# Optimization experiments

Hardware: AMD Instinct MI355X
Metric: run time of the kernel (lower is better)

Reference implementation:

```python
import jax, jax.numpy as jnp
import numpy as np

B, C, H, W = 4, 64, 224, 224
MAX_SEG = 256       # max superpixel label -> segment buffer size 257
MAX_SEG_REF = 256


def _superfeatures(feat, labels, num_seg):
    """scatter_max segment pooling over interior pixels.
    feat [B,C,H,W], labels [B,1,H,W] int -> [B,C,num_seg]."""
    b, c = feat.shape[:2]
    src = feat[:, :, 1:-1, 1:-1].reshape(b, c, -1)   # [B,C,P]
    idx = labels[:, 0, 1:-1, 1:-1].reshape(b, -1)    # [B,P]

    def one(s, i):
        m = jax.ops.segment_max(s.T, i, num_segments=num_seg)  # [S,C]
        return jnp.where(jnp.isneginf(m), 0.0, m).T            # empty segments -> 0

    return jax.vmap(one)(src, idx)                   # [B,C,S]


def _chan_norm(x, eps=1e-5):
    # per-superpixel: subtract channel mean, divide by channel L2 norm (torch dim=1)
    xm = x - jnp.mean(x, axis=1, keepdims=True)
    return xm / (jnp.linalg.norm(xm, axis=1, keepdims=True) + eps)


def setup_inputs():
    key = jax.random.key(0)
    ks = jax.random.split(key, 11)
    rn = lambda k, sh: jax.random.normal(k, sh, dtype=jnp.float32)
    return {
        "feat_target": rn(ks[0], (B, C, H, W)),
        "feat_ref": rn(ks[1], (B, C, H, W)),
        "feat_rgb_ref": rn(ks[2], (B, C, H, W)),
        "Wq": rn(ks[3], (C, C)) * 0.1, "bq": rn(ks[4], (C,)) * 0.1,
        "Wk": rn(ks[5], (C, C)) * 0.1, "bk": rn(ks[6], (C,)) * 0.1,
        "Wv": rn(ks[7], (C, C)) * 0.1, "bv": rn(ks[8], (C,)) * 0.1,
        "label_mask_target": jax.random.randint(ks[9], (B, 1, H, W), 0, MAX_SEG + 1, dtype=jnp.int32),
        "label_mask_ref": jax.random.randint(ks[10], (B, 1, H, W), 0, MAX_SEG_REF + 1, dtype=jnp.int32),
        "max_segments": MAX_SEG,
        "max_segments_ref": MAX_SEG_REF,
    }


def reference(feat_target, feat_ref, feat_rgb_ref, Wq, bq, Wk, bk, Wv, bv,
              label_mask_target, label_mask_ref, max_segments, max_segments_ref):
    S_t = max_segments + 1
    S_r = max_segments_ref + 1
    b, c, h, w = feat_target.shape

    # Superfeatures: segment pooling (scatter_max)
    enc_t = _superfeatures(feat_target, label_mask_target, S_t)   # [B,C,S_t]
    enc_r = _superfeatures(feat_ref, label_mask_ref, S_r)         # [B,C,S_r]
    enc_v = _superfeatures(feat_rgb_ref, label_mask_ref, S_r)     # [B,C,S_r]

    # per-sample variable lengths (label_target / label_ref in the torch loop)
    n_t = jnp.max(label_mask_target.reshape(b, -1), axis=1) + 1
    n_r = jnp.max(label_mask_ref.reshape(b, -1), axis=1) + 1
    tmask = jnp.arange(S_t)[None, :] < n_t[:, None]               # [B,S_t]
    rmask = jnp.arange(S_r)[None, :] < n_r[:, None]               # [B,S_r]

    # Superattention_conv (batched over the original per-sample loop)
    q = jnp.einsum('oc,bcn->bon', Wq, _chan_norm(enc_t)) + bq[None, :, None]
    k = jnp.einsum('oc,bcm->bom', Wk, _chan_norm(enc_r)) + bk[None, :, None]
    v = jnp.einsum('oc,bcm->bom', Wv, enc_v) + bv[None, :, None]  # value conv on raw rgb feats

    sim = jnp.einsum('bcn,bcm->bnm', q, k) / 0.01                 # temperature 0.01
    sim = jnp.where(rmask[:, None, :], sim, -jnp.inf)             # mask invalid ref cols
    attn = jax.nn.softmax(sim, axis=2) * tmask[:, :, None]        # softmax dim=2, zero pad rows

    wg = jnp.einsum('bnm,bcm->bcn', attn, v)                      # [B,C,S_t] (transposed wg_ref)

    # Unpool_features: gather back to pixel grid
    idx = jnp.broadcast_to(label_mask_target.reshape(b, 1, -1), (b, c, h * w))
    unpool = jnp.take_along_axis(wg, idx, axis=2).reshape(b, c, h, w)
    return unpool
```

## Files before the change

### kernel.cpp

```cpp
#include <hip/hip_runtime.h>
#include <math.h>

#define BB 4
#define CC 64
#define HH 224
#define WW 224
#define HWW (HH*WW)
#define SS 257
#define CPB 8
#define NRC 16
#define RPC 14
#define ENCW (3*BB*CC*SS)

__device__ __forceinline__ unsigned fkey(float f) {
    unsigned u = __float_as_uint(f);
    return (u & 0x80000000u) ? ~u : (u | 0x80000000u);
}
__device__ __forceinline__ float funkey(unsigned k) {
    return (k & 0x80000000u) ? __uint_as_float(k & 0x7FFFFFFFu) : __uint_as_float(~k);
}
#define SENT 0x007FFFFFu

__global__ __launch_bounds__(256) void init_kernel(unsigned* __restrict__ enc,
                                                   int* __restrict__ nmax) {
    int i = blockIdx.x * 256 + threadIdx.x;
    if (i < ENCW / 4) ((uint4*)enc)[i] = make_uint4(SENT, SENT, SENT, SENT);
    if (i < 2 * BB) nmax[i] = 0;
}

__global__ __launch_bounds__(256) void pool_kernel(
    const float* __restrict__ fT, const float* __restrict__ fR,
    const float* __restrict__ fV,
    const int* __restrict__ labT, const int* __restrict__ labR,
    unsigned* __restrict__ enc, int* __restrict__ nmax)
{
    __shared__ unsigned seg[CPB * SS];
    __shared__ int wmax[4];
    const int cg = blockIdx.x, rc = blockIdx.y;
    const int z = blockIdx.z >> 2, b = blockIdx.z & 3;
    const float* src = (z == 0) ? fT : (z == 1) ? fR : fV;
    const int*   lab = (z == 0) ? labT : labR;

    for (int i = threadIdx.x; i < CPB * SS; i += 256) seg[i] = SENT;
    __syncthreads();

    const int h0 = rc * RPC;
    const int h1 = min(222, h0 + RPC);
    const int ngroups = (h1 - h0) * 56;

    const int*    lp  = lab + (size_t)b * HWW;
    const int4*   lp4 = (const int4*)lp;
    const float4* fp4 = (const float4*)(src + (size_t)(b * CC + cg * CPB) * HWW);
    const int PS4 = HWW / 4;

    const bool do_nmax = (cg == 0) && (z < 2);
    int lmax = -1;

    for (int gi = threadIdx.x; gi < ngroups; gi += 256) {
        int h = gi / 56;
        int g = gi - h * 56;
        int idx4 = (h0 + h + 1) * 56 + g;
        int4   l  = lp4[idx4];
        float4 f0 = fp4[idx4          ];
        float4 f1 = fp4[idx4 + 1 * PS4];
        float4 f2 = fp4[idx4 + 2 * PS4];
        float4 f3 = fp4[idx4 + 3 * PS4];
        float4 f4 = fp4[idx4 + 4 * PS4];
        float4 f5 = fp4[idx4 + 5 * PS4];
        float4 f6 = fp4[idx4 + 6 * PS4];
        float4 f7 = fp4[idx4 + 7 * PS4];
        if (do_nmax)
            lmax = max(lmax, max(max(l.x, l.y), max(l.z, l.w)));
        const bool mx = (g != 0), mw = (g != 55);
#define PROC(F, CCN) do { \
        unsigned kx = fkey(F.x), ky = fkey(F.y), kz = fkey(F.z), kw = fkey(F.w); \
        unsigned* sg = seg + (CCN) * SS; \
        if (mx && kx > sg[l.x]) atomicMax(&sg[l.x], kx); \
        if (ky > sg[l.y]) atomicMax(&sg[l.y], ky); \
        if (kz > sg[l.z]) atomicMax(&sg[l.z], kz); \
        if (mw && kw > sg[l.w]) atomicMax(&sg[l.w], kw); } while (0)
        PROC(f0, 0); PROC(f1, 1); PROC(f2, 2); PROC(f3, 3);
        PROC(f4, 4); PROC(f5, 5); PROC(f6, 6); PROC(f7, 7);
#undef PROC
    }

    if (do_nmax && threadIdx.x < 56) {
        if (rc == 0) {
            int4 l = lp4[threadIdx.x];
            lmax = max(lmax, max(max(l.x, l.y), max(l.z, l.w)));
        }
        if (rc == NRC - 1) {
            int4 l = lp4[223 * 56 + threadIdx.x];
            lmax = max(lmax, max(max(l.x, l.y), max(l.z, l.w)));
        }
    }
    #pragma unroll
    for (int o = 32; o; o >>= 1) lmax = max(lmax, __shfl_xor(lmax, o, 64));
    if ((threadIdx.x & 63) == 0) wmax[threadIdx.x >> 6] = lmax;
    __syncthreads();
    if (do_nmax && threadIdx.x == 0) {
        int m = max(max(wmax[0], wmax[1]), max(wmax[2], wmax[3]));
        atomicMax(&nmax[z * BB + b], m + 1);
    }

    unsigned* gp = enc + (size_t)((z * BB + b) * CC + cg * CPB) * SS;
    for (int i = threadIdx.x; i < CPB * SS; i += 256) {
        unsigned k = seg[i];
        if (k != SENT) atomicMax(&gp[i], k);
    }
}

__global__ __launch_bounds__(512) void qkv_kernel(
    const unsigned* __restrict__ enc,
    const float* __restrict__ Wq, const float* __restrict__ bq,
    const float* __restrict__ Wk, const float* __restrict__ bk,
    const float* __restrict__ Wv, const float* __restrict__ bv,
    float* __restrict__ qkv)
{
    const int z = blockIdx.z, b = blockIdx.y;
    const int wid = threadIdx.x >> 6, lane = threadIdx.x & 63;
    const int n = blockIdx.x * 8 + wid;
    if (n >= SS) return;

    const float* Wm = (z == 0) ? Wq : (z == 1) ? Wk : Wv;
    const float* bm = (z == 0) ? bq : (z == 1) ? bk : bv;
    const unsigned* ep = enc + (size_t)((z * BB + b) * CC) * SS + n;

    unsigned kraw = ep[(size_t)lane * SS];
    float x = (kraw == SENT) ? 0.0f : funkey(kraw);
    if (z != 2) {
        float s = x;
        for (int o = 32; o; o >>= 1) s += __shfl_xor(s, o, 64);
        float xm = x - s * (1.0f / 64.0f);
        float s2 = xm * xm;
        for (int o = 32; o; o >>= 1) s2 += __shfl_xor(s2, o, 64);
        x = xm / (sqrtf(s2) + 1e-5f);
    }
    float acc = bm[lane];
    #pragma unroll
    for (int cI = 0; cI < 64; ++cI) {
        float xc = __shfl(x, cI, 64);
        acc = fmaf(Wm[lane * 64 + cI], xc, acc);
    }
    qkv[(size_t)((z * BB + b) * SS + n) * CC + lane] = acc;
}

__global__ __launch_bounds__(256) void attn_kernel(
    const float* __restrict__ qkv, const int* __restrict__ nmax,
    float* __restrict__ wg)
{
    const int n = blockIdx.x, b = blockIdx.y, t = threadIdx.x;
    __shared__ float qs[CC];
    __shared__ float sim[512];
    __shared__ float red[256];
    __shared__ float pv[4][64];

    const int nT = nmax[b], nR = nmax[BB + b];
    float* wp = wg + (size_t)(b * SS + n) * CC;
    if (n >= nT) {
        if (t < CC) wp[t] = 0.0f;
        return;
    }
    const float* q = qkv + (size_t)(0 * BB + b) * SS * CC;
    const float* k = qkv + (size_t)(1 * BB + b) * SS * CC;
    const float* v = qkv + (size_t)(2 * BB + b) * SS * CC;

    if (t < CC) qs[t] = q[(size_t)n * CC + t];
    sim[t] = -INFINITY;
    sim[t + 256] = -INFINITY;
    __syncthreads();

    for (int m = t; m < SS; m += 256) {
        float s = -INFINITY;
        if (m < nR) {
            const float4* kr = (const float4*)(k + (size_t)m * CC);
            float acc = 0.0f;
            #pragma unroll
            for (int i = 0; i < 16; ++i) {
                float4 kv = kr[i];
                acc += qs[4*i+0]*kv.x + qs[4*i+1]*kv.y + qs[4*i+2]*kv.z + qs[4*i+3]*kv.w;
            }
            s = acc * 100.0f;
        }
        sim[m] = s;
    }
    __syncthreads();

    red[t] = fmaxf(sim[t], sim[t + 256]);
    __syncthreads();
    for (int s = 128; s > 0; s >>= 1) {
        if (t < s) red[t] = fmaxf(red[t], red[t + s]);
        __syncthreads();
    }
    const float mx = red[0];
    __syncthreads();

    float psum = 0.0f;
    for (int m = t; m < SS; m += 256) {
        float e = expf(sim[m] - mx);
        sim[m] = e;
        psum += e;
    }
    red[t] = psum;
    __syncthreads();
    for (int s = 128; s > 0; s >>= 1) {
        if (t < s) red[t] += red[t + s];
        __syncthreads();
    }
    const float rdenom = 1.0f / red[0];

    const int g = t >> 6, c = t & 63;
    float acc = 0.0f;
    for (int m = g; m < SS; m += 4)
        acc = fmaf(sim[m], v[(size_t)m * CC + c], acc);
    pv[g][c] = acc;
    __syncthreads();
    if (t < CC)
        wp[t] = (pv[0][t] + pv[1][t] + pv[2][t] + pv[3][t]) * rdenom;
}

__global__ __launch_bounds__(256) void unpool_kernel(
    const float* __restrict__ wg, const int* __restrict__ labT,
    float* __restrict__ out)
{
    const int idx = blockIdx.x * 256 + threadIdx.x;
    if (idx >= BB * HWW) return;
    const int b = idx / HWW, hw = idx - b * HWW;
    const int l = labT[idx];
    const float4* row = (const float4*)(wg + (size_t)(b * SS + l) * CC);
    float* op = out + (size_t)b * CC * HWW + hw;
    #pragma unroll
    for (int i = 0; i < 16; ++i) {
        float4 r = row[i];
        op[(size_t)(4*i+0) * HWW] = r.x;
        op[(size_t)(4*i+1) * HWW] = r.y;
        op[(size_t)(4*i+2) * HWW] = r.z;
        op[(size_t)(4*i+3) * HWW] = r.w;
    }
}

extern "C" void kernel_launch(void* const* d_in, const int* in_sizes, int n_in,
                              void* d_out, int out_size, void* d_ws, size_t ws_size,
                              hipStream_t stream) {
    (void)in_sizes; (void)n_in; (void)out_size; (void)ws_size;
    const float* fT  = (const float*)d_in[0];
    const float* fR  = (const float*)d_in[1];
    const float* fV  = (const float*)d_in[2];
    const float* Wq  = (const float*)d_in[3];
    const float* bq  = (const float*)d_in[4];
    const float* Wk  = (const float*)d_in[5];
    const float* bk  = (const float*)d_in[6];
    const float* Wv  = (const float*)d_in[7];
    const float* bv  = (const float*)d_in[8];
    const int* labT  = (const int*)d_in[9];
    const int* labR  = (const int*)d_in[10];
    float* out = (float*)d_out;

    unsigned* enc = (unsigned*)d_ws;
    float* qkv  = (float*)d_ws + ENCW;
    float* wg   = qkv + 3 * BB * CC * SS;
    int*   nmax = (int*)(wg + BB * CC * SS);

    init_kernel<<<(ENCW / 4 + 255) / 256, 256, 0, stream>>>(enc, nmax);
    pool_kernel<<<dim3(CPB, NRC, 12), 256, 0, stream>>>(fT, fR, fV, labT, labR, enc, nmax);
    qkv_kernel<<<dim3((SS + 7) / 8, BB, 3), 512, 0, stream>>>(enc, Wq, bq, Wk, bk, Wv, bv, qkv);
    attn_kernel<<<dim3(SS, BB), 256, 0, stream>>>(qkv, nmax, wg);
    unpool_kernel<<<(BB * HWW + 255) / 256, 256, 0, stream>>>(wg, labT, out);
}
```

Measured before the change: 94.35 us.

## Double-buffer pool loads with inline asm global loads and vmcnt waits

Rewrites the pooling loop as a fixed four-iteration, double-buffered pipeline. Two register sets are filled by inline-asm global_load_dwordx4 using scalar base pointers, and partial s_waitcnt vmcnt lets the next batch of loads stay in flight while the current one runs the shared-memory atomic max. Out-of-range groups are clamped to the last valid group, and the border label reads for nmax are issued before the barrier so they overlap the shared-memory init. This costs more VGPRs, which may lower occupancy, and the inline asm adds fragility.

```diff
diff --git a/kernel.cpp b/kernel.cpp
--- a/kernel.cpp
+++ b/kernel.cpp
@@ -12,6 +12,9 @@
 #define RPC 14
 #define ENCW (3*BB*CC*SS)
 
+typedef float f32x4 __attribute__((ext_vector_type(4)));
+typedef int   i32x4 __attribute__((ext_vector_type(4)));
+
 __device__ __forceinline__ unsigned fkey(float f) {
     unsigned u = __float_as_uint(f);
     return (u & 0x80000000u) ? ~u : (u | 0x80000000u);
@@ -27,6 +30,58 @@
     if (i < ENCW / 4) ((uint4*)enc)[i] = make_uint4(SENT, SENT, SENT, SENT);
     if (i < 2 * BB) nmax[i] = 0;
 }
+
+#define SETA aF0,aF1,aF2,aF3,aF4,aF5,aF6,aF7,aL
+#define SETB bF0,bF1,bF2,bF3,bF4,bF5,bF6,bF7,bL
+
+#define ISSUE_(OFF, F0,F1,F2,F3,F4,F5,F6,F7,LL) \
+    asm volatile( \
+        "global_load_dwordx4 %0, %9, %10\n\t" \
+        "global_load_dwordx4 %1, %9, %11\n\t" \
+        "global_load_dwordx4 %2, %9, %12\n\t" \
+        "global_load_dwordx4 %3, %9, %13\n\t" \
+        "global_load_dwordx4 %4, %9, %14\n\t" \
+        "global_load_dwordx4 %5, %9, %15\n\t" \
+        "global_load_dwordx4 %6, %9, %16\n\t" \
+        "global_load_dwordx4 %7, %9, %17\n\t" \
+        "global_load_dwordx4 %8, %9, %18\n\t" \
+        : "=&v"(F0), "=&v"(F1), "=&v"(F2), "=&v"(F3), \
+          "=&v"(F4), "=&v"(F5), "=&v"(F6), "=&v"(F7), "=&v"(LL) \
+        : "v"(OFF), "s"(q0), "s"(q1), "s"(q2), "s"(q3), \
+          "s"(q4), "s"(q5), "s"(q6), "s"(q7), "s"(ql))
+#define ISSUE(OFF, SET) ISSUE_(OFF, SET)
+
+#define WAITB_(NSTR, F0,F1,F2,F3,F4,F5,F6,F7,LL) \
+    asm volatile("s_waitcnt vmcnt(" NSTR ")" \
+        : "+v"(F0), "+v"(F1), "+v"(F2), "+v"(F3), \
+          "+v"(F4), "+v"(F5), "+v"(F6), "+v"(F7), "+v"(LL))
+#define WAITB(NSTR, SET) WAITB_(NSTR, SET)
+
+#define PR1(F, J, LX, LY, LZ, LW, MX, MW) do { \
+    unsigned kx = fkey(F[0]), ky = fkey(F[1]), kz = fkey(F[2]), kw = fkey(F[3]); \
+    unsigned* sg = seg + (J) * SS; \
+    if ((MX) && kx > sg[LX]) atomicMax(&sg[LX], kx); \
+    if (ky > sg[LY]) atomicMax(&sg[LY], ky); \
+    if (kz > sg[LZ]) atomicMax(&sg[LZ], kz); \
+    if ((MW) && kw > sg[LW]) atomicMax(&sg[LW], kw); \
+} while (0)
+
+#define PROCB_(IT, F0,F1,F2,F3,F4,F5,F6,F7,LL) do { \
+    int gi = min((IT) * 256 + t, NGR - 1); \
+    int g  = gi % 56; \
+    bool mx = (g != 0), mw = (g != 55); \
+    if (do_nmax) lmax = max(lmax, max(max(LL[0], LL[1]), max(LL[2], LL[3]))); \
+    int lx = LL[0], ly = LL[1], lz = LL[2], lw = LL[3]; \
+    PR1(F0, 0, lx, ly, lz, lw, mx, mw); \
+    PR1(F1, 1, lx, ly, lz, lw, mx, mw); \
+    PR1(F2, 2, lx, ly, lz, lw, mx, mw); \
+    PR1(F3, 3, lx, ly, lz, lw, mx, mw); \
+    PR1(F4, 4, lx, ly, lz, lw, mx, mw); \
+    PR1(F5, 5, lx, ly, lz, lw, mx, mw); \
+    PR1(F6, 6, lx, ly, lz, lw, mx, mw); \
+    PR1(F7, 7, lx, ly, lz, lw, mx, mw); \
+} while (0)
+#define PROCB(IT, SET) PROCB_(IT, SET)
 
 __global__ __launch_bounds__(256) void pool_kernel(
     const float* __restrict__ fT, const float* __restrict__ fR,
@@ -38,73 +93,66 @@
     __shared__ int wmax[4];
     const int cg = blockIdx.x, rc = blockIdx.y;
     const int z = blockIdx.z >> 2, b = blockIdx.z & 3;
+    const int t = threadIdx.x;
     const float* src = (z == 0) ? fT : (z == 1) ? fR : fV;
     const int*   lab = (z == 0) ? labT : labR;
 
-    for (int i = threadIdx.x; i < CPB * SS; i += 256) seg[i] = SENT;
-    __syncthreads();
-
-    const int h0 = rc * RPC;
-    const int h1 = min(222, h0 + RPC);
-    const int ngroups = (h1 - h0) * 56;
-
-    const int*    lp  = lab + (size_t)b * HWW;
-    const int4*   lp4 = (const int4*)lp;
-    const float4* fp4 = (const float4*)(src + (size_t)(b * CC + cg * CPB) * HWW);
-    const int PS4 = HWW / 4;
+    const float* pf = src + (size_t)(b * CC + cg * CPB) * HWW;
+    const int*   lp = lab + (size_t)b * HWW;
+    unsigned long long q0 = (unsigned long long)(uintptr_t)(pf + 0 * HWW);
+    unsigned long long q1 = (unsigned long long)(uintptr_t)(pf + 1 * HWW);
+    unsigned long long q2 = (unsigned long long)(uintptr_t)(pf + 2 * HWW);
+    unsigned long long q3 = (unsigned long long)(uintptr_t)(pf + 3 * HWW);
+    unsigned long long q4 = (unsigned long long)(uintptr_t)(pf + 4 * HWW);
+    unsigned long long q5 = (unsigned long long)(uintptr_t)(pf + 5 * HWW);
+    unsigned long long q6 = (unsigned long long)(uintptr_t)(pf + 6 * HWW);
+    unsigned long long q7 = (unsigned long long)(uintptr_t)(pf + 7 * HWW);
+    unsigned long long ql = (unsigned long long)(uintptr_t)lp;
+
+    for (int i = t; i < CPB * SS; i += 256) seg[i] = SENT;
 
     const bool do_nmax = (cg == 0) && (z < 2);
     int lmax = -1;
-
-    for (int gi = threadIdx.x; gi < ngroups; gi += 256) {
-        int h = gi / 56;
-        int g = gi - h * 56;
-        int idx4 = (h0 + h + 1) * 56 + g;
-        int4   l  = lp4[idx4];
-        float4 f0 = fp4[idx4          ];
-        float4 f1 = fp4[idx4 + 1 * PS4];
-        float4 f2 = fp4[idx4 + 2 * PS4];
-        float4 f3 = fp4[idx4 + 3 * PS4];
-        float4 f4 = fp4[idx4 + 4 * PS4];
-        float4 f5 = fp4[idx4 + 5 * PS4];
-        float4 f6 = fp4[idx4 + 6 * PS4];
-        float4 f7 = fp4[idx4 + 7 * PS4];
-        if (do_nmax)
-            lmax = max(lmax, max(max(l.x, l.y), max(l.z, l.w)));
-        const bool mx = (g != 0), mw = (g != 55);
-#define PROC(F, CCN) do { \
-        unsigned kx = fkey(F.x), ky = fkey(F.y), kz = fkey(F.z), kw = fkey(F.w); \
-        unsigned* sg = seg + (CCN) * SS; \
-        if (mx && kx > sg[l.x]) atomicMax(&sg[l.x], kx); \
-        if (ky > sg[l.y]) atomicMax(&sg[l.y], ky); \
-        if (kz > sg[l.z]) atomicMax(&sg[l.z], kz); \
-        if (mw && kw > sg[l.w]) atomicMax(&sg[l.w], kw); } while (0)
-        PROC(f0, 0); PROC(f1, 1); PROC(f2, 2); PROC(f3, 3);
-        PROC(f4, 4); PROC(f5, 5); PROC(f6, 6); PROC(f7, 7);
-#undef PROC
-    }
-
-    if (do_nmax && threadIdx.x < 56) {
-        if (rc == 0) {
-            int4 l = lp4[threadIdx.x];
-            lmax = max(lmax, max(max(l.x, l.y), max(l.z, l.w)));
-        }
-        if (rc == NRC - 1) {
-            int4 l = lp4[223 * 56 + threadIdx.x];
-            lmax = max(lmax, max(max(l.x, l.y), max(l.z, l.w)));
-        }
-    }
+    if (do_nmax && t < 112) {
+        const i32x4* l4 = (const i32x4*)lp;
+        i32x4 v = (t < 56) ? l4[t] : l4[223 * 56 + (t - 56)];
+        lmax = max(lmax, max(max(v[0], v[1]), max(v[2], v[3])));
+    }
+    __syncthreads();
+
+    const int h0i = rc * RPC;
+    const int NGR = (min(222, h0i + RPC) - h0i) * 56;
+    const unsigned base4 = (unsigned)((h0i + 1) * 56);
+
+    f32x4 aF0, aF1, aF2, aF3, aF4, aF5, aF6, aF7; i32x4 aL;
+    f32x4 bF0, bF1, bF2, bF3, bF4, bF5, bF6, bF7; i32x4 bL;
+
+    unsigned vo0 = (base4 + (unsigned)min(0 * 256 + t, NGR - 1)) * 16u;
+    unsigned vo1 = (base4 + (unsigned)min(1 * 256 + t, NGR - 1)) * 16u;
+    unsigned vo2 = (base4 + (unsigned)min(2 * 256 + t, NGR - 1)) * 16u;
+    unsigned vo3 = (base4 + (unsigned)min(3 * 256 + t, NGR - 1)) * 16u;
+
+    ISSUE(vo0, SETA);
+    ISSUE(vo1, SETB);  WAITB("9", SETA);
+    PROCB(0, SETA);
+    ISSUE(vo2, SETA);  WAITB("9", SETB);
+    PROCB(1, SETB);
+    ISSUE(vo3, SETB);  WAITB("9", SETA);
+    PROCB(2, SETA);
+    WAITB("0", SETB);
+    PROCB(3, SETB);
+
     #pragma unroll
     for (int o = 32; o; o >>= 1) lmax = max(lmax, __shfl_xor(lmax, o, 64));
-    if ((threadIdx.x & 63) == 0) wmax[threadIdx.x >> 6] = lmax;
-    __syncthreads();
-    if (do_nmax && threadIdx.x == 0) {
+    if ((t & 63) == 0) wmax[t >> 6] = lmax;
+    __syncthreads();
+    if (do_nmax && t == 0) {
         int m = max(max(wmax[0], wmax[1]), max(wmax[2], wmax[3]));
         atomicMax(&nmax[z * BB + b], m + 1);
     }
 
     unsigned* gp = enc + (size_t)((z * BB + b) * CC + cg * CPB) * SS;
-    for (int i = threadIdx.x; i < CPB * SS; i += 256) {
+    for (int i = t; i < CPB * SS; i += 256) {
         unsigned k = seg[i];
         if (k != SENT) atomicMax(&gp[i], k);
     }
@@ -262,7 +310,7 @@
     int*   nmax = (int*)(wg + BB * CC * SS);
 
     init_kernel<<<(ENCW / 4 + 255) / 256, 256, 0, stream>>>(enc, nmax);
-    pool_kernel<<<dim3(CPB, NRC, 12), 256, 0, stream>>>(fT, fR, fV, labT, labR, enc, nmax);
+    pool_kernel<<<dim3(CC / CPB, NRC, 12), 256, 0, stream>>>(fT, fR, fV, labT, labR, enc, nmax);
     qkv_kernel<<<dim3((SS + 7) / 8, BB, 3), 512, 0, stream>>>(enc, Wq, bq, Wk, bk, Wv, bv, qkv);
     attn_kernel<<<dim3(SS, BB), 256, 0, stream>>>(qkv, nmax, wg);
     unpool_kernel<<<(BB * HWW + 255) / 256, 256, 0, stream>>>(wg, labT, out);
```

Measured after the change: 95.10 us. Within noise of the previous version (+0.8%).
